# Kernel optimization log

Hardware: AMD Instinct MI355X
Metric: run time of the kernel (lower is better)

The kernel has to match this reference:

```python
import jax, jax.numpy as jnp
import numpy as np

N, E, F_IN, HID, HEADS, NT, B = 50000, 400000, 32, 64, 4, 20, 64
IN1 = F_IN + HID  # 96, conv1 input dim after concat with node-type embedding


def _glorot(key, shape):
    fan_in = shape[0]
    return jax.random.normal(key, shape, dtype=jnp.float32) / np.sqrt(fan_in)


def setup_inputs() -> dict:
    key = jax.random.key(0)
    ks = jax.random.split(key, 40)
    inp = {
        "x": jax.random.normal(ks[0], (N, F_IN), dtype=jnp.float32),
        "edge_index": jax.random.randint(ks[1], (2, E), 0, N, dtype=jnp.int32),
        "edge_attr": jax.random.normal(ks[2], (E,), dtype=jnp.float32),
        "batch": jnp.sort(jax.random.randint(ks[3], (N,), 0, B, dtype=jnp.int32)),
        "node_type": jax.random.randint(ks[4], (N,), 0, NT, dtype=jnp.int32),
        # parameters
        "node_emb": jax.random.normal(ks[5], (NT, HID), dtype=jnp.float32) * 0.1,
        "edge_W": _glorot(ks[6], (1, HID)), "edge_b": jnp.zeros((HID,), jnp.float32),
        # GATConv 1 (in=96, out=64, heads=4, edge_dim=64, concat=False)
        "W1": _glorot(ks[7], (IN1, HEADS * HID)),
        "att_src1": jax.random.normal(ks[8], (HEADS, HID), jnp.float32) * 0.1,
        "att_dst1": jax.random.normal(ks[9], (HEADS, HID), jnp.float32) * 0.1,
        "We1": _glorot(ks[10], (HID, HEADS * HID)),
        "att_e1": jax.random.normal(ks[11], (HEADS, HID), jnp.float32) * 0.1,
        "b1": jnp.zeros((HID,), jnp.float32),
        # GATConv 2 (in=64)
        "W2": _glorot(ks[12], (HID, HEADS * HID)),
        "att_src2": jax.random.normal(ks[13], (HEADS, HID), jnp.float32) * 0.1,
        "att_dst2": jax.random.normal(ks[14], (HEADS, HID), jnp.float32) * 0.1,
        "We2": _glorot(ks[15], (HID, HEADS * HID)),
        "att_e2": jax.random.normal(ks[16], (HEADS, HID), jnp.float32) * 0.1,
        "b2": jnp.zeros((HID,), jnp.float32),
        # SAGEConv (mean aggr): out = mean_agg @ Wl + x @ Wr + b
        "sage_Wl": _glorot(ks[17], (HID, HID)), "sage_Wr": _glorot(ks[18], (HID, HID)),
        "sage_b": jnp.zeros((HID,), jnp.float32),
        "lin1_W": _glorot(ks[19], (HID, HID)), "lin1_b": jnp.zeros((HID,), jnp.float32),
        "lin2_W": _glorot(ks[20], (HID, HID)), "lin2_b": jnp.zeros((HID,), jnp.float32),
        "tel_W": _glorot(ks[21], (HID, 1)), "tel_b": jnp.zeros((1,), jnp.float32),
        "comp_W": _glorot(ks[22], (HID, 1)), "comp_b": jnp.zeros((1,), jnp.float32),
        "pch_W": _glorot(ks[23], (HID, 1)), "pch_b": jnp.zeros((1,), jnp.float32),
    }
    return inp


def _gat(x, src, dst, edge_h, W, att_s, att_d, We, att_e, b):
    n = x.shape[0]
    h = (x @ W).reshape(n, HEADS, HID)                       # [N,H,C]
    a_s = (h * att_s).sum(-1)                                # [N,H]
    a_d = (h * att_d).sum(-1)
    e = (edge_h @ We).reshape(-1, HEADS, HID)                # [E,H,C]
    a_e = (e * att_e).sum(-1)                                # [E,H]
    alpha = jax.nn.leaky_relu(a_s[src] + a_d[dst] + a_e, 0.2)
    m = jax.ops.segment_max(alpha, dst, num_segments=n)
    m = jnp.where(jnp.isfinite(m), m, 0.0)
    ex = jnp.exp(alpha - m[dst])
    den = jax.ops.segment_sum(ex, dst, num_segments=n)
    alpha = ex / (den[dst] + 1e-16)                          # segment softmax per dst
    out = jax.ops.segment_sum(h[src] * alpha[..., None], dst, num_segments=n)
    return out.mean(axis=1) + b                              # concat=False -> head mean


def reference(x, edge_index, edge_attr, batch, node_type, node_emb, edge_W, edge_b,
              W1, att_src1, att_dst1, We1, att_e1, b1,
              W2, att_src2, att_dst2, We2, att_e2, b2,
              sage_Wl, sage_Wr, sage_b, lin1_W, lin1_b, lin2_W, lin2_b,
              tel_W, tel_b, comp_W, comp_b, pch_W, pch_b):
    src, dst = edge_index[0], edge_index[1]
    edge_h = edge_attr[:, None] @ edge_W + edge_b            # [E,HID]
    h = jnp.concatenate([x, node_emb[node_type]], axis=-1)   # [N,96]
    h = jax.nn.elu(_gat(h, src, dst, edge_h, W1, att_src1, att_dst1, We1, att_e1, b1))
    h = jax.nn.elu(_gat(h, src, dst, edge_h, W2, att_src2, att_dst2, We2, att_e2, b2))
    # SAGEConv with mean aggregation
    deg = jax.ops.segment_sum(jnp.ones((src.shape[0],), h.dtype), dst, num_segments=N)
    agg = jax.ops.segment_sum(h[src], dst, num_segments=N) / jnp.maximum(deg, 1.0)[:, None]
    h = jax.nn.elu(agg @ sage_Wl + h @ sage_Wr + sage_b)
    # global mean pool over graphs
    cnt = jax.ops.segment_sum(jnp.ones((N,), h.dtype), batch, num_segments=B)
    g = jax.ops.segment_sum(h, batch, num_segments=B) / jnp.maximum(cnt, 1.0)[:, None]
    g = jax.nn.elu(g @ lin1_W + lin1_b)                      # dropout is identity in eval
    g = g @ lin2_W + lin2_b
    return (g @ tel_W + tel_b, g @ comp_W + comp_b, g @ pch_W + pch_b)
```

## Files before the change

### kernel.cpp

```cpp
#include <hip/hip_runtime.h>
#include <hip/hip_bf16.h>


#define NN 50000
#define NE 400000
#define FIN 32
#define NBATCH 64

typedef __hip_bfloat16 bf16;
typedef short bf16x8 __attribute__((ext_vector_type(8)));
typedef float f32x4 __attribute__((ext_vector_type(4)));

__device__ __forceinline__ float b2f(bf16 v) { return __bfloat162float(v); }
__device__ __forceinline__ float lrelu(float x) { return x > 0.f ? x : 0.2f * x; }
__device__ __forceinline__ float eluf(float x) { return x > 0.f ? x : (expf(x) - 1.f); }

__device__ __forceinline__ float4 f4fma(float s, float4 w, float4 c) {
  c.x = fmaf(s, w.x, c.x); c.y = fmaf(s, w.y, c.y);
  c.z = fmaf(s, w.z, c.z); c.w = fmaf(s, w.w, c.w);
  return c;
}

__device__ __forceinline__ float4 upk4(uint2 u) {
  float4 f;
  f.x = __uint_as_float(u.x << 16);
  f.y = __uint_as_float(u.x & 0xffff0000u);
  f.z = __uint_as_float(u.y << 16);
  f.w = __uint_as_float(u.y & 0xffff0000u);
  return f;
}

__device__ __forceinline__ unsigned short bfbits(float f) {
  bf16 b = __float2bfloat16(f);
  unsigned short u;
  __builtin_memcpy(&u, &b, 2);
  return u;
}
__device__ __forceinline__ float hi_f(unsigned short u) {
  return __uint_as_float((unsigned int)u << 16);
}

__global__ __launch_bounds__(256) void k_pq(
    const float* __restrict__ We1, const float* __restrict__ atte1,
    const float* __restrict__ We2, const float* __restrict__ atte2,
    const float* __restrict__ edgeW, const float* __restrict__ edgeB,
    float* __restrict__ pq) {
  int t = threadIdx.x, h = t >> 6, c = t & 63;
  float sW1 = 0.f, sB1 = 0.f, sW2 = 0.f, sB2 = 0.f;
  for (int j = 0; j < 64; ++j) {
    float w = edgeW[j], b = edgeB[j];
    float we1 = We1[j * 256 + h * 64 + c];
    float we2 = We2[j * 256 + h * 64 + c];
    sW1 += w * we1; sB1 += b * we1;
    sW2 += w * we2; sB2 += b * we2;
  }
  float a1 = atte1[h * 64 + c], a2 = atte2[h * 64 + c];
  float p1 = sW1 * a1, q1 = sB1 * a1, p2 = sW2 * a2, q2 = sB2 * a2;
  for (int o = 32; o; o >>= 1) {
    p1 += __shfl_xor(p1, o); q1 += __shfl_xor(q1, o);
    p2 += __shfl_xor(p2, o); q2 += __shfl_xor(q2, o);
  }
  if (c == 0) { pq[h] = p1; pq[4 + h] = q1; pq[8 + h] = p2; pq[12 + h] = q2; }
}

__global__ void k_hist(const int* __restrict__ dst, int* __restrict__ cnt) {
  int e = blockIdx.x * 256 + threadIdx.x;
  if (e < NE) atomicAdd(&cnt[dst[e]], 1);
}

__global__ __launch_bounds__(1024) void k_scan(const int* __restrict__ cnt,
                                               int* __restrict__ off) {
  __shared__ int wsum[16];
  __shared__ int carry;
  int t = threadIdx.x, lane = t & 63, w = t >> 6;
  if (t == 0) { carry = 0; off[0] = 0; }
  __syncthreads();
  for (int base = 0; base < NN; base += 1024) {
    int idx = base + t;
    int v = (idx < NN) ? cnt[idx] : 0;
    int s = v;
    for (int o = 1; o < 64; o <<= 1) { int u = __shfl_up(s, o); if (lane >= o) s += u; }
    if (lane == 63) wsum[w] = s;
    __syncthreads();
    if (t < 16) {
      int ws = wsum[t];
      for (int o = 1; o < 16; o <<= 1) { int u = __shfl_up(ws, o); if (t >= o) ws += u; }
      wsum[t] = ws;
    }
    __syncthreads();
    int add = carry + (w ? wsum[w - 1] : 0);
    if (idx < NN) off[idx + 1] = add + s;
    __syncthreads();
    if (t == 0) carry += wsum[15];
    __syncthreads();
  }
}

__global__ void k_scatter(const int* __restrict__ src, const int* __restrict__ dst,
                          const float* __restrict__ ea, const int* __restrict__ off,
                          int* __restrict__ cur, int* __restrict__ csr_src,
                          float* __restrict__ csr_ea) {
  int e = blockIdx.x * 256 + threadIdx.x;
  if (e >= NE) return;
  int d = dst[e];
  int slot = off[d] + atomicAdd(&cur[d], 1);
  csr_src[slot] = src[e];
  csr_ea[slot] = ea[e];
}

__global__ __launch_bounds__(256) void k_splitA(
    const float* __restrict__ x, const int* __restrict__ ntype,
    const float* __restrict__ emb, unsigned short* __restrict__ Ah,
    unsigned short* __restrict__ Al) {
  const int total = NN * 96;
  for (int i = blockIdx.x * 256 + threadIdx.x; i < total; i += gridDim.x * 256) {
    int n = i / 96, k = i - n * 96;
    float v = (k < FIN) ? x[n * FIN + k] : emb[ntype[n] * 64 + (k - FIN)];
    unsigned short h = bfbits(v);
    Ah[i] = h;
    Al[i] = bfbits(v - hi_f(h));
  }
}

__global__ __launch_bounds__(256) void k_splitW(
    const float* __restrict__ W1, const float* __restrict__ W2,
    unsigned short* __restrict__ B1h, unsigned short* __restrict__ B1l,
    unsigned short* __restrict__ B2h, unsigned short* __restrict__ B2l) {
  int t = blockIdx.x * 256 + threadIdx.x;
  if (t < 256 * 96) {
    int n = t / 96, k = t - n * 96;
    float v = W1[k * 256 + n];
    unsigned short h = bfbits(v);
    B1h[t] = h; B1l[t] = bfbits(v - hi_f(h));
  }
  if (t < 256 * 64) {
    int n = t >> 6, k = t & 63;
    float v = W2[k * 256 + n];
    unsigned short h = bfbits(v);
    B2h[t] = h; B2l[t] = bfbits(v - hi_f(h));
  }
}

template <int K>
__global__ __launch_bounds__(256) void k_mm_mfma(
    const unsigned short* __restrict__ Ah, const unsigned short* __restrict__ Al,
    const unsigned short* __restrict__ Bh, const unsigned short* __restrict__ Bl,
    const float* __restrict__ atts, const float* __restrict__ attd,
    bf16* __restrict__ hmat, float* __restrict__ as_, float* __restrict__ ad_) {
  int m0 = blockIdx.x * 64;
  int w = threadIdx.x >> 6;
  int lane = threadIdx.x & 63;
  int lr = lane & 15;
  int lc = lane >> 4;
  float attsv[4], attdv[4];
  #pragma unroll
  for (int nt = 0; nt < 4; ++nt) {
    attsv[nt] = atts[w * 64 + nt * 16 + lr];
    attdv[nt] = attd[w * 64 + nt * 16 + lr];
  }
  f32x4 acc[4][4] = {};
  #pragma unroll
  for (int ks = 0; ks < K; ks += 32) {
    int koff = ks + lc * 8;
    bf16x8 ah[4], al[4], bh[4], bl[4];
    #pragma unroll
    for (int mt = 0; mt < 4; ++mt) {
      int m = m0 + mt * 16 + lr;
      if (m > NN - 1) m = NN - 1;
      ah[mt] = *reinterpret_cast<const bf16x8*>(&Ah[(size_t)m * K + koff]);
      al[mt] = *reinterpret_cast<const bf16x8*>(&Al[(size_t)m * K + koff]);
    }
    #pragma unroll
    for (int nt = 0; nt < 4; ++nt) {
      int n = w * 64 + nt * 16 + lr;
      bh[nt] = *reinterpret_cast<const bf16x8*>(&Bh[(size_t)n * K + koff]);
      bl[nt] = *reinterpret_cast<const bf16x8*>(&Bl[(size_t)n * K + koff]);
    }
    #pragma unroll
    for (int mt = 0; mt < 4; ++mt) {
      #pragma unroll
      for (int nt = 0; nt < 4; ++nt) {
        acc[mt][nt] = __builtin_amdgcn_mfma_f32_16x16x32_bf16(ah[mt], bh[nt], acc[mt][nt], 0, 0, 0);
        acc[mt][nt] = __builtin_amdgcn_mfma_f32_16x16x32_bf16(al[mt], bh[nt], acc[mt][nt], 0, 0, 0);
        acc[mt][nt] = __builtin_amdgcn_mfma_f32_16x16x32_bf16(ah[mt], bl[nt], acc[mt][nt], 0, 0, 0);
      }
    }
  }
  #pragma unroll
  for (int mt = 0; mt < 4; ++mt) {
    #pragma unroll
    for (int reg = 0; reg < 4; ++reg) {
      int row = m0 + mt * 16 + lc * 4 + reg;
      float sS = 0.f, sD = 0.f;
      #pragma unroll
      for (int nt = 0; nt < 4; ++nt) {
        float v = acc[mt][nt][reg];
        sS += v * attsv[nt];
        sD += v * attdv[nt];
      }
      for (int o = 1; o < 16; o <<= 1) {
        sS += __shfl_xor(sS, o);
        sD += __shfl_xor(sD, o);
      }
      if (row < NN) {
        #pragma unroll
        for (int nt = 0; nt < 4; ++nt)
          hmat[(size_t)row * 256 + w * 64 + nt * 16 + lr] =
              __float2bfloat16(acc[mt][nt][reg]);
        if (lr == 0) { as_[row * 4 + w] = sS; ad_[row * 4 + w] = sD; }
      }
    }
  }
}

__global__ __launch_bounds__(256) void k_gat(
    const int* __restrict__ off, const int* __restrict__ csr_src,
    const float* __restrict__ csr_ea, const float* __restrict__ as_,
    const float* __restrict__ ad_, const float* __restrict__ pq, int pqo,
    const bf16* __restrict__ hmat, const float* __restrict__ bias,
    float* __restrict__ outf, unsigned short* __restrict__ oph,
    unsigned short* __restrict__ opl) {
  __shared__ float wlds[4][256];
  int wv = threadIdx.x >> 6;
  int wid = (blockIdx.x << 2) + wv;
  int lane = threadIdx.x & 63;
  if (wid >= NN) return;
  int beg = off[wid], end = off[wid + 1];
  int deg = end - beg;
  int hsel = lane >> 4;
  float4 D = reinterpret_cast<const float4*>(ad_)[wid];
  float p0 = pq[pqo + 0], p1 = pq[pqo + 1], p2 = pq[pqo + 2], p3 = pq[pqo + 3];
  float q0 = pq[pqo + 4], q1 = pq[pqo + 5], q2 = pq[pqo + 6], q3 = pq[pqo + 7];
  float4 acc = {0.f, 0.f, 0.f, 0.f};

  if (deg <= 64) {
    bool valid = lane < deg;
    float lx = -INFINITY, ly = -INFINITY, lz = -INFINITY, lw = -INFINITY;
    if (valid) {
      int s = csr_src[beg + lane];
      float ea = csr_ea[beg + lane];
      float4 A = reinterpret_cast<const float4*>(as_)[s];
      lx = lrelu(A.x + D.x + ea * p0 + q0);
      ly = lrelu(A.y + D.y + ea * p1 + q1);
      lz = lrelu(A.z + D.z + ea * p2 + q2);
      lw = lrelu(A.w + D.w + ea * p3 + q3);
    }
    float m0 = lx, m1 = ly, m2 = lz, m3 = lw;
    for (int o = 32; o; o >>= 1) {
      m0 = fmaxf(m0, __shfl_xor(m0, o));
      m1 = fmaxf(m1, __shfl_xor(m1, o));
      m2 = fmaxf(m2, __shfl_xor(m2, o));
      m3 = fmaxf(m3, __shfl_xor(m3, o));
    }
    float w0 = valid ? __expf(lx - m0) : 0.f;
    float w1 = valid ? __expf(ly - m1) : 0.f;
    float w2 = valid ? __expf(lz - m2) : 0.f;
    float w3 = valid ? __expf(lw - m3) : 0.f;
    float s0 = w0, s1 = w1, s2 = w2, s3 = w3;
    for (int o = 32; o; o >>= 1) {
      s0 += __shfl_xor(s0, o); s1 += __shfl_xor(s1, o);
      s2 += __shfl_xor(s2, o); s3 += __shfl_xor(s3, o);
    }
    float4 wv4;
    wv4.x = w0 / (s0 + 1e-16f);
    wv4.y = w1 / (s1 + 1e-16f);
    wv4.z = w2 / (s2 + 1e-16f);
    wv4.w = w3 / (s3 + 1e-16f);
    reinterpret_cast<float4*>(&wlds[wv][0])[lane] = wv4;
    const float* wp = &wlds[wv][0];
    int j = 0;
    for (; j + 4 <= deg; j += 4) {
      int sA = csr_src[beg + j + 0];
      int sB = csr_src[beg + j + 1];
      int sC = csr_src[beg + j + 2];
      int sD = csr_src[beg + j + 3];
      float wA = wp[4 * (j + 0) + hsel];
      float wB = wp[4 * (j + 1) + hsel];
      float wC = wp[4 * (j + 2) + hsel];
      float wD = wp[4 * (j + 3) + hsel];
      uint2 uA = *reinterpret_cast<const uint2*>(&hmat[(size_t)sA * 256 + 4 * lane]);
      uint2 uB = *reinterpret_cast<const uint2*>(&hmat[(size_t)sB * 256 + 4 * lane]);
      uint2 uC = *reinterpret_cast<const uint2*>(&hmat[(size_t)sC * 256 + 4 * lane]);
      uint2 uD = *reinterpret_cast<const uint2*>(&hmat[(size_t)sD * 256 + 4 * lane]);
      acc = f4fma(wA, upk4(uA), acc);
      acc = f4fma(wB, upk4(uB), acc);
      acc = f4fma(wC, upk4(uC), acc);
      acc = f4fma(wD, upk4(uD), acc);
    }
    for (; j < deg; ++j) {
      int s = csr_src[beg + j];
      float w = wp[4 * j + hsel];
      uint2 u = *reinterpret_cast<const uint2*>(&hmat[(size_t)s * 256 + 4 * lane]);
      acc = f4fma(w, upk4(u), acc);
    }
  } else {
    float m0 = -INFINITY, m1 = -INFINITY, m2 = -INFINITY, m3 = -INFINITY;
    float s0 = 0.f, s1 = 0.f, s2 = 0.f, s3 = 0.f;
    for (int e = beg + lane; e < end; e += 64) {
      int s = csr_src[e];
      float ea = csr_ea[e];
      float4 A = reinterpret_cast<const float4*>(as_)[s];
      float lx = lrelu(A.x + D.x + ea * p0 + q0);
      float ly = lrelu(A.y + D.y + ea * p1 + q1);
      float lz = lrelu(A.z + D.z + ea * p2 + q2);
      float lw = lrelu(A.w + D.w + ea * p3 + q3);
      float nm;
      nm = fmaxf(m0, lx); s0 = s0 * __expf(m0 - nm) + __expf(lx - nm); m0 = nm;
      nm = fmaxf(m1, ly); s1 = s1 * __expf(m1 - nm) + __expf(ly - nm); m1 = nm;
      nm = fmaxf(m2, lz); s2 = s2 * __expf(m2 - nm) + __expf(lz - nm); m2 = nm;
      nm = fmaxf(m3, lw); s3 = s3 * __expf(m3 - nm) + __expf(lw - nm); m3 = nm;
    }
    for (int o = 32; o; o >>= 1) {
      float om, os, nm;
      om = __shfl_xor(m0, o); os = __shfl_xor(s0, o); nm = fmaxf(m0, om);
      s0 = s0 * __expf(fmaxf(m0 - nm, -80.f)) + os * __expf(fmaxf(om - nm, -80.f)); m0 = nm;
      om = __shfl_xor(m1, o); os = __shfl_xor(s1, o); nm = fmaxf(m1, om);
      s1 = s1 * __expf(fmaxf(m1 - nm, -80.f)) + os * __expf(fmaxf(om - nm, -80.f)); m1 = nm;
      om = __shfl_xor(m2, o); os = __shfl_xor(s2, o); nm = fmaxf(m2, om);
      s2 = s2 * __expf(fmaxf(m2 - nm, -80.f)) + os * __expf(fmaxf(om - nm, -80.f)); m2 = nm;
      om = __shfl_xor(m3, o); os = __shfl_xor(s3, o); nm = fmaxf(m3, om);
      s3 = s3 * __expf(fmaxf(m3 - nm, -80.f)) + os * __expf(fmaxf(om - nm, -80.f)); m3 = nm;
    }
    float i0 = 1.f / (s0 + 1e-16f), i1 = 1.f / (s1 + 1e-16f);
    float i2 = 1.f / (s2 + 1e-16f), i3 = 1.f / (s3 + 1e-16f);
    float Dh = hsel == 0 ? D.x : hsel == 1 ? D.y : hsel == 2 ? D.z : D.w;
    float ph = hsel == 0 ? p0 : hsel == 1 ? p1 : hsel == 2 ? p2 : p3;
    float qh = hsel == 0 ? q0 : hsel == 1 ? q1 : hsel == 2 ? q2 : q3;
    float mh = hsel == 0 ? m0 : hsel == 1 ? m1 : hsel == 2 ? m2 : m3;
    float ih = hsel == 0 ? i0 : hsel == 1 ? i1 : hsel == 2 ? i2 : i3;
    for (int j = beg; j < end; ++j) {
      int s = csr_src[j];
      float ea = csr_ea[j];
      float4 A = reinterpret_cast<const float4*>(as_)[s];
      float Ah = hsel == 0 ? A.x : hsel == 1 ? A.y : hsel == 2 ? A.z : A.w;
      float l = lrelu(Ah + Dh + ea * ph + qh);
      float w = __expf(l - mh) * ih;
      uint2 u = *reinterpret_cast<const uint2*>(&hmat[(size_t)s * 256 + 4 * lane]);
      acc = f4fma(w, upk4(u), acc);
    }
  }
  acc.x += __shfl_xor(acc.x, 16); acc.y += __shfl_xor(acc.y, 16);
  acc.z += __shfl_xor(acc.z, 16); acc.w += __shfl_xor(acc.w, 16);
  acc.x += __shfl_xor(acc.x, 32); acc.y += __shfl_xor(acc.y, 32);
  acc.z += __shfl_xor(acc.z, 32); acc.w += __shfl_xor(acc.w, 32);
  if (lane < 16) {
    float4 bv = reinterpret_cast<const float4*>(bias)[lane];
    float4 r;
    r.x = eluf(0.25f * acc.x + bv.x);
    r.y = eluf(0.25f * acc.y + bv.y);
    r.z = eluf(0.25f * acc.z + bv.z);
    r.w = eluf(0.25f * acc.w + bv.w);
    if (outf) reinterpret_cast<float4*>(&outf[(size_t)wid * 64])[lane] = r;
    if (oph) {
      ushort4 h4, l4;
      h4.x = bfbits(r.x); l4.x = bfbits(r.x - hi_f(h4.x));
      h4.y = bfbits(r.y); l4.y = bfbits(r.y - hi_f(h4.y));
      h4.z = bfbits(r.z); l4.z = bfbits(r.z - hi_f(h4.z));
      h4.w = bfbits(r.w); l4.w = bfbits(r.w - hi_f(h4.w));
      *reinterpret_cast<ushort4*>(&oph[(size_t)wid * 64 + lane * 4]) = h4;
      *reinterpret_cast<ushort4*>(&opl[(size_t)wid * 64 + lane * 4]) = l4;
    }
  }
}

__global__ __launch_bounds__(256) void k_agg(
    const int* __restrict__ off, const int* __restrict__ csr_src,
    const float* __restrict__ h3, float* __restrict__ agg) {
  int wid = (blockIdx.x << 2) + (threadIdx.x >> 6);
  int lane = threadIdx.x & 63;
  if (wid >= NN) return;
  int beg = off[wid], end = off[wid + 1];
  float acc = 0.f;
  int e = beg;
  for (; e + 4 <= end; e += 4) {
    int s0 = csr_src[e + 0], s1 = csr_src[e + 1];
    int s2 = csr_src[e + 2], s3 = csr_src[e + 3];
    float v0 = h3[(size_t)s0 * 64 + lane];
    float v1 = h3[(size_t)s1 * 64 + lane];
    float v2 = h3[(size_t)s2 * 64 + lane];
    float v3 = h3[(size_t)s3 * 64 + lane];
    acc += (v0 + v1) + (v2 + v3);
  }
  for (; e < end; ++e) acc += h3[(size_t)csr_src[e] * 64 + lane];
  agg[(size_t)wid * 64 + lane] = acc / fmaxf((float)(end - beg), 1.f);
}

__global__ __launch_bounds__(256) void k_sage_mm(
    const float* __restrict__ agg, const float* __restrict__ h3,
    const float* __restrict__ Wl, const float* __restrict__ Wr,
    const float* __restrict__ bias, float* __restrict__ out) {
  __shared__ float WlS[4096];
  __shared__ float WrS[4096];
  __shared__ float Ag[2048];
  __shared__ float Hr[2048];
  int t = threadIdx.x;
  for (int i = t; i < 4096; i += 256) { WlS[i] = Wl[i]; WrS[i] = Wr[i]; }
  int ct = t & 15, rg = t >> 4;
  float4 bv = reinterpret_cast<const float4*>(bias)[ct];
  for (int r0 = blockIdx.x * 32; r0 < NN; r0 += gridDim.x * 32) {
    for (int i = t; i < 2048; i += 256) {
      int n = r0 + (i >> 6);
      float va = 0.f, vh = 0.f;
      if (n < NN) {
        va = agg[(size_t)n * 64 + (i & 63)];
        vh = h3[(size_t)n * 64 + (i & 63)];
      }
      Ag[i] = va; Hr[i] = vh;
    }
    __syncthreads();
    float4 c0 = {0.f, 0.f, 0.f, 0.f}, c1 = c0;
    const float* a0 = &Ag[(rg * 2 + 0) * 64];
    const float* a1 = &Ag[(rg * 2 + 1) * 64];
    const float* h0 = &Hr[(rg * 2 + 0) * 64];
    const float* h1 = &Hr[(rg * 2 + 1) * 64];
    #pragma unroll 4
    for (int k = 0; k < 64; k += 4) {
      float4 wl0 = *reinterpret_cast<const float4*>(&WlS[(k + 0) * 64 + ct * 4]);
      float4 wl1 = *reinterpret_cast<const float4*>(&WlS[(k + 1) * 64 + ct * 4]);
      float4 wl2 = *reinterpret_cast<const float4*>(&WlS[(k + 2) * 64 + ct * 4]);
      float4 wl3 = *reinterpret_cast<const float4*>(&WlS[(k + 3) * 64 + ct * 4]);
      float4 wr0 = *reinterpret_cast<const float4*>(&WrS[(k + 0) * 64 + ct * 4]);
      float4 wr1 = *reinterpret_cast<const float4*>(&WrS[(k + 1) * 64 + ct * 4]);
      float4 wr2 = *reinterpret_cast<const float4*>(&WrS[(k + 2) * 64 + ct * 4]);
      float4 wr3 = *reinterpret_cast<const float4*>(&WrS[(k + 3) * 64 + ct * 4]);
      float4 aa0 = *reinterpret_cast<const float4*>(&a0[k]);
      float4 aa1 = *reinterpret_cast<const float4*>(&a1[k]);
      float4 hh0 = *reinterpret_cast<const float4*>(&h0[k]);
      float4 hh1 = *reinterpret_cast<const float4*>(&h1[k]);
      c0 = f4fma(aa0.x, wl0, c0); c0 = f4fma(aa0.y, wl1, c0);
      c0 = f4fma(aa0.z, wl2, c0); c0 = f4fma(aa0.w, wl3, c0);
      c0 = f4fma(hh0.x, wr0, c0); c0 = f4fma(hh0.y, wr1, c0);
      c0 = f4fma(hh0.z, wr2, c0); c0 = f4fma(hh0.w, wr3, c0);
      c1 = f4fma(aa1.x, wl0, c1); c1 = f4fma(aa1.y, wl1, c1);
      c1 = f4fma(aa1.z, wl2, c1); c1 = f4fma(aa1.w, wl3, c1);
      c1 = f4fma(hh1.x, wr0, c1); c1 = f4fma(hh1.y, wr1, c1);
      c1 = f4fma(hh1.z, wr2, c1); c1 = f4fma(hh1.w, wr3, c1);
    }
    int n0 = r0 + rg * 2;
    if (n0 + 0 < NN) {
      float4 r;
      r.x = eluf(c0.x + bv.x); r.y = eluf(c0.y + bv.y);
      r.z = eluf(c0.z + bv.z); r.w = eluf(c0.w + bv.w);
      *reinterpret_cast<float4*>(&out[(size_t)(n0 + 0) * 64 + ct * 4]) = r;
    }
    if (n0 + 1 < NN) {
      float4 r;
      r.x = eluf(c1.x + bv.x); r.y = eluf(c1.y + bv.y);
      r.z = eluf(c1.z + bv.z); r.w = eluf(c1.w + bv.w);
      *reinterpret_cast<float4*>(&out[(size_t)(n0 + 1) * 64 + ct * 4]) = r;
    }
    __syncthreads();
  }
}

__global__ __launch_bounds__(256) void k_pool2(const float* __restrict__ hs,
                                               const int* __restrict__ batch,
                                               float* __restrict__ g) {
  int cid = (blockIdx.x << 2) + (threadIdx.x >> 6);
  int lane = threadIdx.x & 63;
  int n0 = cid * 32;
  if (n0 >= NN) return;
  int n1 = n0 + 32 < NN ? n0 + 32 : NN;
  int cur = batch[n0];
  float acc = 0.f;
  for (int n = n0; n < n1; ++n) {
    int b = batch[n];
    if (b != cur) {
      atomicAdd(&g[cur * 64 + lane], acc);
      acc = 0.f;
      cur = b;
    }
    acc += hs[(size_t)n * 64 + lane];
  }
  atomicAdd(&g[cur * 64 + lane], acc);
}

__device__ __forceinline__ int lowerb(const int* __restrict__ a, int n, int key) {
  int lo = 0, hi = n;
  while (lo < hi) { int mid = (lo + hi) >> 1; if (a[mid] < key) lo = mid + 1; else hi = mid; }
  return lo;
}

__global__ __launch_bounds__(256) void k_head(
    const float* __restrict__ g, const int* __restrict__ batch,
    const float* __restrict__ l1W, const float* __restrict__ l1b,
    const float* __restrict__ l2W, const float* __restrict__ l2b,
    const float* __restrict__ telW, const float* __restrict__ telb,
    const float* __restrict__ compW, const float* __restrict__ compb,
    const float* __restrict__ pchW, const float* __restrict__ pchb,
    float* __restrict__ out) {
  __shared__ float gS[4096];
  __shared__ float WS[4096];
  __shared__ float hS[4096];
  __shared__ float invc[64];
  int t = threadIdx.x;
  if (t < 64) {
    int lo = lowerb(batch, NN, t), hi = lowerb(batch, NN, t + 1);
    invc[t] = 1.f / fmaxf((float)(hi - lo), 1.f);
  }
  for (int i = t; i < 4096; i += 256) WS[i] = l1W[i];
  __syncthreads();
  for (int i = t; i < 4096; i += 256) gS[i] = g[i] * invc[i >> 6];
  __syncthreads();
  for (int i = t; i < 4096; i += 256) {
    int r = i >> 6, j = i & 63;
    float s = 0.f;
    for (int k = 0; k < 64; ++k) s += gS[r * 64 + k] * WS[k * 64 + j];
    hS[i] = eluf(s + l1b[j]);
  }
  __syncthreads();
  for (int i = t; i < 4096; i += 256) WS[i] = l2W[i];
  __syncthreads();
  for (int i = t; i < 4096; i += 256) {
    int r = i >> 6, j = i & 63;
    float s = 0.f;
    for (int k = 0; k < 64; ++k) s += hS[r * 64 + k] * WS[k * 64 + j];
    gS[i] = s + l2b[j];
  }
  __syncthreads();
  if (t < 192) {
    int head = t >> 6, r = t & 63;
    const float* Wv = head == 0 ? telW : (head == 1 ? compW : pchW);
    float bb = head == 0 ? telb[0] : (head == 1 ? compb[0] : pchb[0]);
    float s = 0.f;
    for (int k = 0; k < 64; ++k) s += gS[r * 64 + k] * Wv[k];
    out[t] = s + bb;
  }
}

extern "C" void kernel_launch(void* const* d_in, const int* in_sizes, int n_in,
                              void* d_out, int out_size, void* d_ws, size_t ws_size,
                              hipStream_t stream) {
  const float* x     = (const float*)d_in[0];
  const int*   eidx  = (const int*)d_in[1];
  const float* eattr = (const float*)d_in[2];
  const int*   batch = (const int*)d_in[3];
  const int*   ntype = (const int*)d_in[4];
  const float* nemb  = (const float*)d_in[5];
  const float* edgeW = (const float*)d_in[6];
  const float* edgeB = (const float*)d_in[7];
  const float* W1    = (const float*)d_in[8];
  const float* atts1 = (const float*)d_in[9];
  const float* attd1 = (const float*)d_in[10];
  const float* We1   = (const float*)d_in[11];
  const float* atte1 = (const float*)d_in[12];
  const float* b1    = (const float*)d_in[13];
  const float* W2    = (const float*)d_in[14];
  const float* atts2 = (const float*)d_in[15];
  const float* attd2 = (const float*)d_in[16];
  const float* We2   = (const float*)d_in[17];
  const float* atte2 = (const float*)d_in[18];
  const float* b2    = (const float*)d_in[19];
  const float* sageWl = (const float*)d_in[20];
  const float* sageWr = (const float*)d_in[21];
  const float* sageB  = (const float*)d_in[22];
  const float* l1W = (const float*)d_in[23];
  const float* l1b = (const float*)d_in[24];
  const float* l2W = (const float*)d_in[25];
  const float* l2b = (const float*)d_in[26];
  const float* telW  = (const float*)d_in[27];
  const float* telb  = (const float*)d_in[28];
  const float* compW = (const float*)d_in[29];
  const float* compb = (const float*)d_in[30];
  const float* pchW  = (const float*)d_in[31];
  const float* pchb  = (const float*)d_in[32];

  char* wp = (char*)d_ws;
  auto alloc = [&](size_t bytes) -> char* {
    char* p = wp;
    wp += (bytes + 255) & ~(size_t)255;
    return p;
  };
  float*  pq      = (float*)alloc(16 * 4);
  int*    cnt     = (int*)alloc((size_t)NN * 4);
  int*    off     = (int*)alloc(((size_t)NN + 1) * 4);
  int*    csr_src = (int*)alloc((size_t)NE * 4);
  float*  csr_ea  = (float*)alloc((size_t)NE * 4);
  float*  as_     = (float*)alloc((size_t)NN * 16);
  float*  ad_     = (float*)alloc((size_t)NN * 16);
  bf16*   hmat    = (bf16*)alloc((size_t)NN * 256 * 2);
  float*  nodeB   = (float*)alloc((size_t)NN * 64 * 4);
  float*  aggbuf  = (float*)alloc((size_t)NN * 64 * 4);
  unsigned short* B1h = (unsigned short*)alloc(256 * 96 * 2);
  unsigned short* B1l = (unsigned short*)alloc(256 * 96 * 2);
  unsigned short* B2h = (unsigned short*)alloc(256 * 64 * 2);
  unsigned short* B2l = (unsigned short*)alloc(256 * 64 * 2);
  char* R = alloc((size_t)NN * 96 * 2 * 2);
  unsigned short* A1h = (unsigned short*)R;
  unsigned short* A1l = A1h + (size_t)NN * 96;
  unsigned short* A2h = (unsigned short*)R;
  unsigned short* A2l = A2h + (size_t)NN * 64;
  float* sageout = (float*)R;
  float* gbuf = (float*)alloc(64 * 64 * 4);

  const int* srcI = eidx;
  const int* dstI = eidx + NE;

  hipMemsetAsync(cnt, 0, (size_t)NN * 4, stream);
  hipMemsetAsync(gbuf, 0, 64 * 64 * 4, stream);
  k_pq<<<1, 256, 0, stream>>>(We1, atte1, We2, atte2, edgeW, edgeB, pq);
  k_hist<<<(NE + 255) / 256, 256, 0, stream>>>(dstI, cnt);
  k_scan<<<1, 1024, 0, stream>>>(cnt, off);
  hipMemsetAsync(cnt, 0, (size_t)NN * 4, stream);
  k_scatter<<<(NE + 255) / 256, 256, 0, stream>>>(srcI, dstI, eattr, off, cnt,
                                                  csr_src, csr_ea);
  k_splitW<<<96, 256, 0, stream>>>(W1, W2, B1h, B1l, B2h, B2l);
  k_splitA<<<2048, 256, 0, stream>>>(x, ntype, nemb, A1h, A1l);
  k_mm_mfma<96><<<(NN + 63) / 64, 256, 0, stream>>>(
      A1h, A1l, B1h, B1l, atts1, attd1, hmat, as_, ad_);
  k_gat<<<NN / 4, 256, 0, stream>>>(off, csr_src, csr_ea, as_, ad_, pq, 0,
                                    hmat, b1, nullptr, A2h, A2l);
  k_mm_mfma<64><<<(NN + 63) / 64, 256, 0, stream>>>(
      A2h, A2l, B2h, B2l, atts2, attd2, hmat, as_, ad_);
  k_gat<<<NN / 4, 256, 0, stream>>>(off, csr_src, csr_ea, as_, ad_, pq, 8,
                                    hmat, b2, nodeB, nullptr, nullptr);
  k_agg<<<NN / 4, 256, 0, stream>>>(off, csr_src, nodeB, aggbuf);
  k_sage_mm<<<1024, 256, 0, stream>>>(aggbuf, nodeB, sageWl, sageWr, sageB,
                                      sageout);
  k_pool2<<<((NN + 31) / 32 + 3) / 4, 256, 0, stream>>>(sageout, batch, gbuf);
  k_head<<<1, 256, 0, stream>>>(gbuf, batch, l1W, l1b, l2W, l2b, telW, telb,
                                compW, compb, pchW, pchb, (float*)d_out);
}
```

Baseline: 468.2 us.

## Parallelize GAT/SAGE neighbor gathers across edges, merge prep kernels, faster scan

In the low-degree GAT path each wave now processes four neighbors at once, one per 16-lane group with 16 features per lane. Source indices are broadcast by shuffle and the partial sums are reduced across groups afterwards; the SAGE mean aggregation gets the same treatment with float4 loads. The two weight-prep kernels merge into one launch. The scan now uses one pass with contiguous chunks per thread, and the scatter counts down the histogram with atomicSub, which drops a memset. Together these cut dependent gather latency, launch count and scan barriers, at the cost of more cross-lane shuffle reductions and lanes left idle when the degree is not a multiple of four.

```diff
diff --git a/kernel.cpp b/kernel.cpp
--- a/kernel.cpp
+++ b/kernel.cpp
@@ -21,12 +21,12 @@
   return c;
 }
 
-__device__ __forceinline__ float4 upk4(uint2 u) {
+__device__ __forceinline__ float4 upk4(unsigned int lo, unsigned int hi) {
   float4 f;
-  f.x = __uint_as_float(u.x << 16);
-  f.y = __uint_as_float(u.x & 0xffff0000u);
-  f.z = __uint_as_float(u.y << 16);
-  f.w = __uint_as_float(u.y & 0xffff0000u);
+  f.x = __uint_as_float(lo << 16);
+  f.y = __uint_as_float(lo & 0xffff0000u);
+  f.z = __uint_as_float(hi << 16);
+  f.w = __uint_as_float(hi & 0xffff0000u);
   return f;
 }
 
@@ -40,27 +40,46 @@
   return __uint_as_float((unsigned int)u << 16);
 }
 
-__global__ __launch_bounds__(256) void k_pq(
+__global__ __launch_bounds__(256) void k_prep(
+    const float* __restrict__ W1, const float* __restrict__ W2,
     const float* __restrict__ We1, const float* __restrict__ atte1,
     const float* __restrict__ We2, const float* __restrict__ atte2,
     const float* __restrict__ edgeW, const float* __restrict__ edgeB,
+    unsigned short* __restrict__ B1h, unsigned short* __restrict__ B1l,
+    unsigned short* __restrict__ B2h, unsigned short* __restrict__ B2l,
     float* __restrict__ pq) {
-  int t = threadIdx.x, h = t >> 6, c = t & 63;
-  float sW1 = 0.f, sB1 = 0.f, sW2 = 0.f, sB2 = 0.f;
-  for (int j = 0; j < 64; ++j) {
-    float w = edgeW[j], b = edgeB[j];
-    float we1 = We1[j * 256 + h * 64 + c];
-    float we2 = We2[j * 256 + h * 64 + c];
-    sW1 += w * we1; sB1 += b * we1;
-    sW2 += w * we2; sB2 += b * we2;
-  }
-  float a1 = atte1[h * 64 + c], a2 = atte2[h * 64 + c];
-  float p1 = sW1 * a1, q1 = sB1 * a1, p2 = sW2 * a2, q2 = sB2 * a2;
-  for (int o = 32; o; o >>= 1) {
-    p1 += __shfl_xor(p1, o); q1 += __shfl_xor(q1, o);
-    p2 += __shfl_xor(p2, o); q2 += __shfl_xor(q2, o);
-  }
-  if (c == 0) { pq[h] = p1; pq[4 + h] = q1; pq[8 + h] = p2; pq[12 + h] = q2; }
+  if (blockIdx.x == 96) {
+    int t = threadIdx.x, h = t >> 6, c = t & 63;
+    float sW1 = 0.f, sB1 = 0.f, sW2 = 0.f, sB2 = 0.f;
+    for (int j = 0; j < 64; ++j) {
+      float w = edgeW[j], b = edgeB[j];
+      float we1 = We1[j * 256 + h * 64 + c];
+      float we2 = We2[j * 256 + h * 64 + c];
+      sW1 += w * we1; sB1 += b * we1;
+      sW2 += w * we2; sB2 += b * we2;
+    }
+    float a1 = atte1[h * 64 + c], a2 = atte2[h * 64 + c];
+    float p1 = sW1 * a1, q1 = sB1 * a1, p2 = sW2 * a2, q2 = sB2 * a2;
+    for (int o = 32; o; o >>= 1) {
+      p1 += __shfl_xor(p1, o); q1 += __shfl_xor(q1, o);
+      p2 += __shfl_xor(p2, o); q2 += __shfl_xor(q2, o);
+    }
+    if (c == 0) { pq[h] = p1; pq[4 + h] = q1; pq[8 + h] = p2; pq[12 + h] = q2; }
+    return;
+  }
+  int t = blockIdx.x * 256 + threadIdx.x;
+  if (t < 256 * 96) {
+    int n = t / 96, k = t - n * 96;
+    float v = W1[k * 256 + n];
+    unsigned short h = bfbits(v);
+    B1h[t] = h; B1l[t] = bfbits(v - hi_f(h));
+  }
+  if (t < 256 * 64) {
+    int n = t >> 6, k = t & 63;
+    float v = W2[k * 256 + n];
+    unsigned short h = bfbits(v);
+    B2h[t] = h; B2l[t] = bfbits(v - hi_f(h));
+  }
 }
 
 __global__ void k_hist(const int* __restrict__ dst, int* __restrict__ cnt) {
@@ -71,39 +90,38 @@
 __global__ __launch_bounds__(1024) void k_scan(const int* __restrict__ cnt,
                                                int* __restrict__ off) {
   __shared__ int wsum[16];
-  __shared__ int carry;
   int t = threadIdx.x, lane = t & 63, w = t >> 6;
-  if (t == 0) { carry = 0; off[0] = 0; }
+  const int PER = (NN + 1023) / 1024;
+  int base = t * PER;
+  int n = NN - base;
+  if (n < 0) n = 0;
+  if (n > PER) n = PER;
+  int s = 0;
+  for (int i = 0; i < n; ++i) s += cnt[base + i];
+  int ps = s;
+  for (int o = 1; o < 64; o <<= 1) { int u = __shfl_up(ps, o); if (lane >= o) ps += u; }
+  if (lane == 63) wsum[w] = ps;
   __syncthreads();
-  for (int base = 0; base < NN; base += 1024) {
-    int idx = base + t;
-    int v = (idx < NN) ? cnt[idx] : 0;
-    int s = v;
-    for (int o = 1; o < 64; o <<= 1) { int u = __shfl_up(s, o); if (lane >= o) s += u; }
-    if (lane == 63) wsum[w] = s;
-    __syncthreads();
-    if (t < 16) {
-      int ws = wsum[t];
-      for (int o = 1; o < 16; o <<= 1) { int u = __shfl_up(ws, o); if (t >= o) ws += u; }
-      wsum[t] = ws;
-    }
-    __syncthreads();
-    int add = carry + (w ? wsum[w - 1] : 0);
-    if (idx < NN) off[idx + 1] = add + s;
-    __syncthreads();
-    if (t == 0) carry += wsum[15];
-    __syncthreads();
-  }
+  if (t < 16) {
+    int ws = wsum[t];
+    for (int o = 1; o < 16; o <<= 1) { int u = __shfl_up(ws, o); if (t >= o) ws += u; }
+    wsum[t] = ws;
+  }
+  __syncthreads();
+  int run = (ps - s) + (w ? wsum[w - 1] : 0);
+  if (t == 0) off[0] = 0;
+  for (int i = 0; i < n; ++i) { run += cnt[base + i]; off[base + i + 1] = run; }
 }
 
 __global__ void k_scatter(const int* __restrict__ src, const int* __restrict__ dst,
                           const float* __restrict__ ea, const int* __restrict__ off,
-                          int* __restrict__ cur, int* __restrict__ csr_src,
+                          int* __restrict__ cnt, int* __restrict__ csr_src,
                           float* __restrict__ csr_ea) {
   int e = blockIdx.x * 256 + threadIdx.x;
   if (e >= NE) return;
   int d = dst[e];
-  int slot = off[d] + atomicAdd(&cur[d], 1);
+  int r = atomicSub(&cnt[d], 1);
+  int slot = off[d] + r - 1;
   csr_src[slot] = src[e];
   csr_ea[slot] = ea[e];
 }
@@ -119,25 +137,6 @@
     unsigned short h = bfbits(v);
     Ah[i] = h;
     Al[i] = bfbits(v - hi_f(h));
-  }
-}
-
-__global__ __launch_bounds__(256) void k_splitW(
-    const float* __restrict__ W1, const float* __restrict__ W2,
-    unsigned short* __restrict__ B1h, unsigned short* __restrict__ B1l,
-    unsigned short* __restrict__ B2h, unsigned short* __restrict__ B2l) {
-  int t = blockIdx.x * 256 + threadIdx.x;
-  if (t < 256 * 96) {
-    int n = t / 96, k = t - n * 96;
-    float v = W1[k * 256 + n];
-    unsigned short h = bfbits(v);
-    B1h[t] = h; B1l[t] = bfbits(v - hi_f(h));
-  }
-  if (t < 256 * 64) {
-    int n = t >> 6, k = t & 63;
-    float v = W2[k * 256 + n];
-    unsigned short h = bfbits(v);
-    B2h[t] = h; B2l[t] = bfbits(v - hi_f(h));
   }
 }
 
@@ -227,19 +226,18 @@
   if (wid >= NN) return;
   int beg = off[wid], end = off[wid + 1];
   int deg = end - beg;
-  int hsel = lane >> 4;
   float4 D = reinterpret_cast<const float4*>(ad_)[wid];
   float p0 = pq[pqo + 0], p1 = pq[pqo + 1], p2 = pq[pqo + 2], p3 = pq[pqo + 3];
   float q0 = pq[pqo + 4], q1 = pq[pqo + 5], q2 = pq[pqo + 6], q3 = pq[pqo + 7];
-  float4 acc = {0.f, 0.f, 0.f, 0.f};
 
   if (deg <= 64) {
     bool valid = lane < deg;
+    int se = 0;
     float lx = -INFINITY, ly = -INFINITY, lz = -INFINITY, lw = -INFINITY;
     if (valid) {
-      int s = csr_src[beg + lane];
+      se = csr_src[beg + lane];
       float ea = csr_ea[beg + lane];
-      float4 A = reinterpret_cast<const float4*>(as_)[s];
+      float4 A = reinterpret_cast<const float4*>(as_)[se];
       lx = lrelu(A.x + D.x + ea * p0 + q0);
       ly = lrelu(A.y + D.y + ea * p1 + q1);
       lz = lrelu(A.z + D.z + ea * p2 + q2);
@@ -267,33 +265,69 @@
     wv4.z = w2 / (s2 + 1e-16f);
     wv4.w = w3 / (s3 + 1e-16f);
     reinterpret_cast<float4*>(&wlds[wv][0])[lane] = wv4;
+    int grp = lane >> 4, cl = lane & 15;
+    int hsl = cl >> 2;
     const float* wp = &wlds[wv][0];
-    int j = 0;
-    for (; j + 4 <= deg; j += 4) {
-      int sA = csr_src[beg + j + 0];
-      int sB = csr_src[beg + j + 1];
-      int sC = csr_src[beg + j + 2];
-      int sD = csr_src[beg + j + 3];
-      float wA = wp[4 * (j + 0) + hsel];
-      float wB = wp[4 * (j + 1) + hsel];
-      float wC = wp[4 * (j + 2) + hsel];
-      float wD = wp[4 * (j + 3) + hsel];
-      uint2 uA = *reinterpret_cast<const uint2*>(&hmat[(size_t)sA * 256 + 4 * lane]);
-      uint2 uB = *reinterpret_cast<const uint2*>(&hmat[(size_t)sB * 256 + 4 * lane]);
-      uint2 uC = *reinterpret_cast<const uint2*>(&hmat[(size_t)sC * 256 + 4 * lane]);
-      uint2 uD = *reinterpret_cast<const uint2*>(&hmat[(size_t)sD * 256 + 4 * lane]);
-      acc = f4fma(wA, upk4(uA), acc);
-      acc = f4fma(wB, upk4(uB), acc);
-      acc = f4fma(wC, upk4(uC), acc);
-      acc = f4fma(wD, upk4(uD), acc);
-    }
-    for (; j < deg; ++j) {
-      int s = csr_src[beg + j];
-      float w = wp[4 * j + hsel];
-      uint2 u = *reinterpret_cast<const uint2*>(&hmat[(size_t)s * 256 + 4 * lane]);
-      acc = f4fma(w, upk4(u), acc);
+    float4 a0 = {0.f, 0.f, 0.f, 0.f}, a1 = a0, a2 = a0, a3 = a0;
+    for (int jb = 0; jb < deg; jb += 4) {
+      int j = jb + grp;
+      if (j < deg) {
+        int s = __shfl(se, j);
+        float w = wp[4 * j + hsl];
+        const bf16* hp = &hmat[(size_t)s * 256 + cl * 16];
+        uint4 u0 = *reinterpret_cast<const uint4*>(hp);
+        uint4 u1 = *reinterpret_cast<const uint4*>(hp + 8);
+        a0 = f4fma(w, upk4(u0.x, u0.y), a0);
+        a1 = f4fma(w, upk4(u0.z, u0.w), a1);
+        a2 = f4fma(w, upk4(u1.x, u1.y), a2);
+        a3 = f4fma(w, upk4(u1.z, u1.w), a3);
+      }
+    }
+    #pragma unroll
+    for (int o = 4; o <= 32; o <<= 1) {
+      a0.x += __shfl_xor(a0.x, o); a0.y += __shfl_xor(a0.y, o);
+      a0.z += __shfl_xor(a0.z, o); a0.w += __shfl_xor(a0.w, o);
+      a1.x += __shfl_xor(a1.x, o); a1.y += __shfl_xor(a1.y, o);
+      a1.z += __shfl_xor(a1.z, o); a1.w += __shfl_xor(a1.w, o);
+      a2.x += __shfl_xor(a2.x, o); a2.y += __shfl_xor(a2.y, o);
+      a2.z += __shfl_xor(a2.z, o); a2.w += __shfl_xor(a2.w, o);
+      a3.x += __shfl_xor(a3.x, o); a3.y += __shfl_xor(a3.y, o);
+      a3.z += __shfl_xor(a3.z, o); a3.w += __shfl_xor(a3.w, o);
+    }
+    if (lane < 4) {
+      float4 rr0 = a0, rr1 = a1, rr2 = a2, rr3 = a3;
+      float4 b0 = reinterpret_cast<const float4*>(bias)[lane * 4 + 0];
+      float4 b1v = reinterpret_cast<const float4*>(bias)[lane * 4 + 1];
+      float4 b2v = reinterpret_cast<const float4*>(bias)[lane * 4 + 2];
+      float4 b3v = reinterpret_cast<const float4*>(bias)[lane * 4 + 3];
+      rr0.x = eluf(0.25f * rr0.x + b0.x); rr0.y = eluf(0.25f * rr0.y + b0.y);
+      rr0.z = eluf(0.25f * rr0.z + b0.z); rr0.w = eluf(0.25f * rr0.w + b0.w);
+      rr1.x = eluf(0.25f * rr1.x + b1v.x); rr1.y = eluf(0.25f * rr1.y + b1v.y);
+      rr1.z = eluf(0.25f * rr1.z + b1v.z); rr1.w = eluf(0.25f * rr1.w + b1v.w);
+      rr2.x = eluf(0.25f * rr2.x + b2v.x); rr2.y = eluf(0.25f * rr2.y + b2v.y);
+      rr2.z = eluf(0.25f * rr2.z + b2v.z); rr2.w = eluf(0.25f * rr2.w + b2v.w);
+      rr3.x = eluf(0.25f * rr3.x + b3v.x); rr3.y = eluf(0.25f * rr3.y + b3v.y);
+      rr3.z = eluf(0.25f * rr3.z + b3v.z); rr3.w = eluf(0.25f * rr3.w + b3v.w);
+      if (outf) {
+        float4* o = reinterpret_cast<float4*>(&outf[(size_t)wid * 64 + lane * 16]);
+        o[0] = rr0; o[1] = rr1; o[2] = rr2; o[3] = rr3;
+      }
+      if (oph) {
+        float4 rr[4] = {rr0, rr1, rr2, rr3};
+        #pragma unroll
+        for (int i = 0; i < 4; ++i) {
+          ushort4 h4, l4;
+          h4.x = bfbits(rr[i].x); l4.x = bfbits(rr[i].x - hi_f(h4.x));
+          h4.y = bfbits(rr[i].y); l4.y = bfbits(rr[i].y - hi_f(h4.y));
+          h4.z = bfbits(rr[i].z); l4.z = bfbits(rr[i].z - hi_f(h4.z));
+          h4.w = bfbits(rr[i].w); l4.w = bfbits(rr[i].w - hi_f(h4.w));
+          *reinterpret_cast<ushort4*>(&oph[(size_t)wid * 64 + lane * 16 + i * 4]) = h4;
+          *reinterpret_cast<ushort4*>(&opl[(size_t)wid * 64 + lane * 16 + i * 4]) = l4;
+        }
+      }
     }
   } else {
+    int hsel = lane >> 4;
     float m0 = -INFINITY, m1 = -INFINITY, m2 = -INFINITY, m3 = -INFINITY;
     float s0 = 0.f, s1 = 0.f, s2 = 0.f, s3 = 0.f;
     for (int e = beg + lane; e < end; e += 64) {
@@ -328,6 +362,7 @@
     float qh = hsel == 0 ? q0 : hsel == 1 ? q1 : hsel == 2 ? q2 : q3;
     float mh = hsel == 0 ? m0 : hsel == 1 ? m1 : hsel == 2 ? m2 : m3;
     float ih = hsel == 0 ? i0 : hsel == 1 ? i1 : hsel == 2 ? i2 : i3;
+    float4 acc = {0.f, 0.f, 0.f, 0.f};
     for (int j = beg; j < end; ++j) {
       int s = csr_src[j];
       float ea = csr_ea[j];
@@ -336,29 +371,29 @@
       float l = lrelu(Ah + Dh + ea * ph + qh);
       float w = __expf(l - mh) * ih;
       uint2 u = *reinterpret_cast<const uint2*>(&hmat[(size_t)s * 256 + 4 * lane]);
-      acc = f4fma(w, upk4(u), acc);
-    }
-  }
-  acc.x += __shfl_xor(acc.x, 16); acc.y += __shfl_xor(acc.y, 16);
-  acc.z += __shfl_xor(acc.z, 16); acc.w += __shfl_xor(acc.w, 16);
-  acc.x += __shfl_xor(acc.x, 32); acc.y += __shfl_xor(acc.y, 32);
-  acc.z += __shfl_xor(acc.z, 32); acc.w += __shfl_xor(acc.w, 32);
-  if (lane < 16) {
-    float4 bv = reinterpret_cast<const float4*>(bias)[lane];
-    float4 r;
-    r.x = eluf(0.25f * acc.x + bv.x);
-    r.y = eluf(0.25f * acc.y + bv.y);
-    r.z = eluf(0.25f * acc.z + bv.z);
-    r.w = eluf(0.25f * acc.w + bv.w);
-    if (outf) reinterpret_cast<float4*>(&outf[(size_t)wid * 64])[lane] = r;
-    if (oph) {
-      ushort4 h4, l4;
-      h4.x = bfbits(r.x); l4.x = bfbits(r.x - hi_f(h4.x));
-      h4.y = bfbits(r.y); l4.y = bfbits(r.y - hi_f(h4.y));
-      h4.z = bfbits(r.z); l4.z = bfbits(r.z - hi_f(h4.z));
-      h4.w = bfbits(r.w); l4.w = bfbits(r.w - hi_f(h4.w));
-      *reinterpret_cast<ushort4*>(&oph[(size_t)wid * 64 + lane * 4]) = h4;
-      *reinterpret_cast<ushort4*>(&opl[(size_t)wid * 64 + lane * 4]) = l4;
+      acc = f4fma(w, upk4(u.x, u.y), acc);
+    }
+    acc.x += __shfl_xor(acc.x, 16); acc.y += __shfl_xor(acc.y, 16);
+    acc.z += __shfl_xor(acc.z, 16); acc.w += __shfl_xor(acc.w, 16);
+    acc.x += __shfl_xor(acc.x, 32); acc.y += __shfl_xor(acc.y, 32);
+    acc.z += __shfl_xor(acc.z, 32); acc.w += __shfl_xor(acc.w, 32);
+    if (lane < 16) {
+      float4 bv = reinterpret_cast<const float4*>(bias)[lane];
+      float4 r;
+      r.x = eluf(0.25f * acc.x + bv.x);
+      r.y = eluf(0.25f * acc.y + bv.y);
+      r.z = eluf(0.25f * acc.z + bv.z);
+      r.w = eluf(0.25f * acc.w + bv.w);
+      if (outf) reinterpret_cast<float4*>(&outf[(size_t)wid * 64])[lane] = r;
+      if (oph) {
+        ushort4 h4, l4;
+        h4.x = bfbits(r.x); l4.x = bfbits(r.x - hi_f(h4.x));
+        h4.y = bfbits(r.y); l4.y = bfbits(r.y - hi_f(h4.y));
+        h4.z = bfbits(r.z); l4.z = bfbits(r.z - hi_f(h4.z));
+        h4.w = bfbits(r.w); l4.w = bfbits(r.w - hi_f(h4.w));
+        *reinterpret_cast<ushort4*>(&oph[(size_t)wid * 64 + lane * 4]) = h4;
+        *reinterpret_cast<ushort4*>(&opl[(size_t)wid * 64 + lane * 4]) = l4;
+      }
     }
   }
 }
@@ -370,19 +405,35 @@
   int lane = threadIdx.x & 63;
   if (wid >= NN) return;
   int beg = off[wid], end = off[wid + 1];
-  float acc = 0.f;
-  int e = beg;
-  for (; e + 4 <= end; e += 4) {
-    int s0 = csr_src[e + 0], s1 = csr_src[e + 1];
-    int s2 = csr_src[e + 2], s3 = csr_src[e + 3];
-    float v0 = h3[(size_t)s0 * 64 + lane];
-    float v1 = h3[(size_t)s1 * 64 + lane];
-    float v2 = h3[(size_t)s2 * 64 + lane];
-    float v3 = h3[(size_t)s3 * 64 + lane];
-    acc += (v0 + v1) + (v2 + v3);
-  }
-  for (; e < end; ++e) acc += h3[(size_t)csr_src[e] * 64 + lane];
-  agg[(size_t)wid * 64 + lane] = acc / fmaxf((float)(end - beg), 1.f);
+  int deg = end - beg;
+  if (deg <= 64) {
+    int se = (lane < deg) ? csr_src[beg + lane] : 0;
+    int grp = lane >> 4, cl = lane & 15;
+    float4 acc = {0.f, 0.f, 0.f, 0.f};
+    for (int jb = 0; jb < deg; jb += 4) {
+      int j = jb + grp;
+      if (j < deg) {
+        int s = __shfl(se, j);
+        float4 v = *reinterpret_cast<const float4*>(&h3[(size_t)s * 64 + cl * 4]);
+        acc.x += v.x; acc.y += v.y; acc.z += v.z; acc.w += v.w;
+      }
+    }
+    #pragma unroll
+    for (int o = 16; o <= 32; o <<= 1) {
+      acc.x += __shfl_xor(acc.x, o); acc.y += __shfl_xor(acc.y, o);
+      acc.z += __shfl_xor(acc.z, o); acc.w += __shfl_xor(acc.w, o);
+    }
+    if (lane < 16) {
+      float inv = 1.f / fmaxf((float)deg, 1.f);
+      float4 r;
+      r.x = acc.x * inv; r.y = acc.y * inv; r.z = acc.z * inv; r.w = acc.w * inv;
+      reinterpret_cast<float4*>(&agg[(size_t)wid * 64])[cl] = r;
+    }
+  } else {
+    float acc = 0.f;
+    for (int e = beg; e < end; ++e) acc += h3[(size_t)csr_src[e] * 64 + lane];
+    agg[(size_t)wid * 64 + lane] = acc / fmaxf((float)deg, 1.f);
+  }
 }
 
 __global__ __launch_bounds__(256) void k_sage_mm(
@@ -598,13 +649,12 @@
 
   hipMemsetAsync(cnt, 0, (size_t)NN * 4, stream);
   hipMemsetAsync(gbuf, 0, 64 * 64 * 4, stream);
-  k_pq<<<1, 256, 0, stream>>>(We1, atte1, We2, atte2, edgeW, edgeB, pq);
+  k_prep<<<97, 256, 0, stream>>>(W1, W2, We1, atte1, We2, atte2, edgeW, edgeB,
+                                 B1h, B1l, B2h, B2l, pq);
   k_hist<<<(NE + 255) / 256, 256, 0, stream>>>(dstI, cnt);
   k_scan<<<1, 1024, 0, stream>>>(cnt, off);
-  hipMemsetAsync(cnt, 0, (size_t)NN * 4, stream);
   k_scatter<<<(NE + 255) / 256, 256, 0, stream>>>(srcI, dstI, eattr, off, cnt,
                                                   csr_src, csr_ea);
-  k_splitW<<<96, 256, 0, stream>>>(W1, W2, B1h, B1l, B2h, B2l);
   k_splitA<<<2048, 256, 0, stream>>>(x, ntype, nemb, A1h, A1l);
   k_mm_mfma<96><<<(NN + 63) / 64, 256, 0, stream>>>(
       A1h, A1l, B1h, B1l, atts1, attd1, hmat, as_, ad_);
```

New measurement: 534.0 us. 14.1% more time.
